# Kernel optimization log

Hardware: AMD Instinct MI355X
Metric: run time of the kernel (lower is better)

Reference implementation:

```python
import jax, jax.numpy as jnp
import numpy as np

N = 100000
C = 32            # channels per degree (shape_in == shape_out == 32)
NI = C * C        # flattened Gram-matrix size = n_input = n_hidden
LN_EPS = 1e-5
SLOPE = 0.01      # LeakyReLU default negative slope


def _ln(x, g, b):
    mu = jnp.mean(x, axis=-1, keepdims=True)
    var = jnp.var(x, axis=-1, keepdims=True)  # biased, matches torch LayerNorm
    return (x - mu) * jax.lax.rsqrt(var + LN_EPS) * g + b


def _lrelu(x):
    return jnp.where(x >= 0, x, SLOPE * x)


def _gal(v, g1, b1, w1, g2, b2, w2, bias2):
    # v: [N, ch_in, m]
    n, ci, _ = v.shape
    dot = jnp.einsum('nac,nbc->nab', v, v).reshape(n, ci * ci)  # Gram matrix
    dot = jnp.sign(dot) * jnp.maximum(jnp.abs(dot), 1e-12)
    h = _lrelu(_ln(dot, g1, b1)) @ w1.T           # [N, ch_in*ch_out]
    h = _lrelu(_ln(h, g2, b2)) @ w2.T + bias2      # [N, ch_in*ch_out]
    attn = jax.nn.softmax(h.reshape(n, -1, ci), axis=-1)  # [N, ch_out, ch_in]
    return jnp.einsum('nab,nbc->nac', attn, v)     # [N, ch_out, m]


def _mk_type_params(key):
    ks = jax.random.split(key, 3)
    bound = np.sqrt(6.0 / NI)  # kaiming_uniform_, fan_in=NI
    return dict(
        ln1_g=jnp.ones((NI,), jnp.float32),
        ln1_b=jnp.zeros((NI,), jnp.float32),
        w1=jax.random.uniform(ks[0], (NI, NI), jnp.float32, -bound, bound),
        ln2_g=jnp.ones((NI,), jnp.float32),
        ln2_b=jnp.zeros((NI,), jnp.float32),
        w2=jax.random.uniform(ks[1], (NI, NI), jnp.float32, -bound, bound),
        b2=jax.random.uniform(ks[2], (NI,), jnp.float32, -1.0 / C, 1.0 / C),
    )


def setup_inputs():
    key = jax.random.key(0)
    k0, k1, kp0, kp1 = jax.random.split(key, 4)
    d = {
        'f0': jax.random.normal(k0, (N, C, 1), jnp.float32),
        'f1': jax.random.normal(k1, (N, C, 3), jnp.float32),
    }
    for tag, kk in (('0', kp0), ('1', kp1)):
        p = _mk_type_params(kk)
        for name, val in p.items():
            d[f'{name}_{tag}'] = val
    return d


def reference(f0, f1,
              ln1_g_0, ln1_b_0, w1_0, ln2_g_0, ln2_b_0, w2_0, b2_0,
              ln1_g_1, ln1_b_1, w1_1, ln2_g_1, ln2_b_1, w2_1, b2_1):
    out0 = _gal(f0, ln1_g_0, ln1_b_0, w1_0, ln2_g_0, ln2_b_0, w2_0, b2_0)
    out1 = _gal(f1, ln1_g_1, ln1_b_1, w1_1, ln2_g_1, ln2_b_1, w2_1, b2_1)
    return (out0, out1)
```

## Files before the change

### kernel.cpp

```cpp
#include <hip/hip_runtime.h>

#define NN     100000
#define NB     1563
#define LN_EPS 1e-5f
#define SLOPE  0.01f

typedef __bf16 bf16x8 __attribute__((ext_vector_type(8)));
typedef float  f32x4  __attribute__((ext_vector_type(4)));
typedef unsigned short u16;
typedef unsigned int   u32;

union Pack8 { uint4 u4; bf16x8 bf; u16 s[8]; };

__device__ __forceinline__ u16 f2bf(float x){
    u32 b = __float_as_uint(x);
    b += 0x7fffu + ((b >> 16) & 1u);
    return (u16)(b >> 16);
}
__device__ __forceinline__ float bf2f(u32 s){
    return __uint_as_float(s << 16);
}

__global__ __launch_bounds__(1024) void prep_weights(
    const float* __restrict__ wa, const float* __restrict__ wb,
    const float* __restrict__ wc, const float* __restrict__ wd,
    u16* __restrict__ dst)
{
    int m = blockIdx.y;
    const float* src = (m==0)? wa : (m==1)? wb : (m==2)? wc : wd;
    u16* d = dst + (size_t)m * (1024u*1024u);
    int tid = blockIdx.x * blockDim.x + threadIdx.x;
    int sub = tid & 3;
    int row = (tid >> 2) & 1023;
    int kb  = tid >> 12;
    const float4* s4 = (const float4*)(src + row*1024 + kb*32 + sub*8);
    float4 a = s4[0], b = s4[1];
    Pack8 p;
    p.s[0]=f2bf(a.x); p.s[1]=f2bf(a.y); p.s[2]=f2bf(a.z); p.s[3]=f2bf(a.w);
    p.s[4]=f2bf(b.x); p.s[5]=f2bf(b.y); p.s[6]=f2bf(b.z); p.s[7]=f2bf(b.w);
    ((uint4*)d)[(kb*1024 + row)*4 + sub] = p.u4;
}

__device__ __forceinline__ void gemm_quad(
    const u16* __restrict__ Wp, const u16* xs,
    int wv, int lane15, int q, f32x4 acc[4][4])
{
    const uint4* bA = (const uint4*)Wp + (wv*32 + lane15)*4 + q;
    const uint4* bB = (const uint4*)Wp + ((wv+16)*32 + lane15)*4 + q;
    const uint4* ab = (const uint4*)xs + q*64 + lane15;
    #pragma unroll
    for (int ct=0; ct<4; ++ct)
      #pragma unroll
      for (int rt=0; rt<4; ++rt)
        acc[ct][rt] = (f32x4){0.f,0.f,0.f,0.f};
    #pragma unroll 2
    for (int ks=0; ks<32; ++ks){
        Pack8 b0, b1, b2, b3, a0, a1, a2, a3;
        b0.u4 = bA[ks*4096];
        b1.u4 = bA[ks*4096 + 64];
        b2.u4 = bB[ks*4096];
        b3.u4 = bB[ks*4096 + 64];
        a0.u4 = ab[ks*256];
        a1.u4 = ab[ks*256 + 16];
        a2.u4 = ab[ks*256 + 32];
        a3.u4 = ab[ks*256 + 48];
        acc[0][0] = __builtin_amdgcn_mfma_f32_16x16x32_bf16(a0.bf, b0.bf, acc[0][0], 0,0,0);
        acc[0][1] = __builtin_amdgcn_mfma_f32_16x16x32_bf16(a1.bf, b0.bf, acc[0][1], 0,0,0);
        acc[0][2] = __builtin_amdgcn_mfma_f32_16x16x32_bf16(a2.bf, b0.bf, acc[0][2], 0,0,0);
        acc[0][3] = __builtin_amdgcn_mfma_f32_16x16x32_bf16(a3.bf, b0.bf, acc[0][3], 0,0,0);
        acc[1][0] = __builtin_amdgcn_mfma_f32_16x16x32_bf16(a0.bf, b1.bf, acc[1][0], 0,0,0);
        acc[1][1] = __builtin_amdgcn_mfma_f32_16x16x32_bf16(a1.bf, b1.bf, acc[1][1], 0,0,0);
        acc[1][2] = __builtin_amdgcn_mfma_f32_16x16x32_bf16(a2.bf, b1.bf, acc[1][2], 0,0,0);
        acc[1][3] = __builtin_amdgcn_mfma_f32_16x16x32_bf16(a3.bf, b1.bf, acc[1][3], 0,0,0);
        acc[2][0] = __builtin_amdgcn_mfma_f32_16x16x32_bf16(a0.bf, b2.bf, acc[2][0], 0,0,0);
        acc[2][1] = __builtin_amdgcn_mfma_f32_16x16x32_bf16(a1.bf, b2.bf, acc[2][1], 0,0,0);
        acc[2][2] = __builtin_amdgcn_mfma_f32_16x16x32_bf16(a2.bf, b2.bf, acc[2][2], 0,0,0);
        acc[2][3] = __builtin_amdgcn_mfma_f32_16x16x32_bf16(a3.bf, b2.bf, acc[2][3], 0,0,0);
        acc[3][0] = __builtin_amdgcn_mfma_f32_16x16x32_bf16(a0.bf, b3.bf, acc[3][0], 0,0,0);
        acc[3][1] = __builtin_amdgcn_mfma_f32_16x16x32_bf16(a1.bf, b3.bf, acc[3][1], 0,0,0);
        acc[3][2] = __builtin_amdgcn_mfma_f32_16x16x32_bf16(a2.bf, b3.bf, acc[3][2], 0,0,0);
        acc[3][3] = __builtin_amdgcn_mfma_f32_16x16x32_bf16(a3.bf, b3.bf, acc[3][3], 0,0,0);
    }
}

template<int MDIM>
__global__ __launch_bounds__(1024, 4) void gal_fused(
    const float* __restrict__ f,
    const float* __restrict__ ln1g, const float* __restrict__ ln1b,
    const float* __restrict__ ln2g, const float* __restrict__ ln2b,
    const float* __restrict__ b2,
    const u16* __restrict__ Wp1, const u16* __restrict__ Wp2,
    float* __restrict__ outp)
{
    extern __shared__ char smem[];
    constexpr int VSTR = 32*MDIM + 4;
    constexpr int SBS  = 64*32 + 4;
    u16*   xs    = (u16*)smem;
    float* sbuf  = (float*)smem;
    float* vbuf  = (float*)smem + 32832;
    float* stats = (float*)smem + 32832 + 64*VSTR;

    const int tid    = threadIdx.x;
    const int lane   = tid & 63;
    const int wv     = tid >> 6;
    const int lane15 = lane & 15;
    const int q      = lane >> 4;
    const int node0  = blockIdx.x * 64;

    if (tid < 128) stats[tid] = 0.f;
    {
        const int gbase = node0*32*MDIM;
        for (int i = tid; i < 64*32*MDIM; i += 1024){
            int nd = i / (32*MDIM);
            int r  = i - nd*(32*MDIM);
            float val = (gbase + i < NN*32*MDIM) ? f[gbase + i] : 0.f;
            vbuf[nd*VSTR + r] = val;
        }
    }
    __syncthreads();

    {
        const int n = tid >> 4;
        const int j = tid & 15;
        const float* vn = vbuf + n*VSTR;
        float va[2][MDIM];
        #pragma unroll
        for (int c=0;c<MDIM;++c){ va[0][c]=vn[(j*2)*MDIM+c]; va[1][c]=vn[(j*2+1)*MDIM+c]; }
        float sum=0.f, ssum=0.f;
        #pragma unroll
        for (int b=0;b<32;++b){
            float d0=0.f, d1=0.f;
            #pragma unroll
            for (int c=0;c<MDIM;++c){ float vb = vn[b*MDIM+c]; d0 += va[0][c]*vb; d1 += va[1][c]*vb; }
            sum += d0+d1; ssum += d0*d0 + d1*d1;
        }
        #pragma unroll
        for (int st=1; st<16; st<<=1){ sum += __shfl_xor(sum, st); ssum += __shfl_xor(ssum, st); }
        float mu   = sum * (1.f/1024.f);
        float rstd = rsqrtf(ssum*(1.f/1024.f) - mu*mu + LN_EPS);
        #pragma unroll
        for (int jb=0;jb<8;++jb){
            Pack8 p;
            const int ai = jb >> 2;
            #pragma unroll
            for (int l=0;l<8;++l){
                int b = (jb*8+l) & 31;
                float d = 0.f;
                #pragma unroll
                for (int c=0;c<MDIM;++c) d += va[ai][c]*vn[b*MDIM+c];
                int k = j*64 + jb*8 + l;
                float x = (d - mu)*rstd*ln1g[k] + ln1b[k];
                x = (x >= 0.f)? x : SLOPE*x;
                p.s[l] = f2bf(x);
            }
            ((uint4*)xs)[(j*8+jb)*64 + n] = p.u4;
        }
    }
    __syncthreads();

    u32 h1pk[4][4][2];
    {
        f32x4 acc[4][4];
        gemm_quad(Wp1, xs, wv, lane15, q, acc);
        float p_[16], pp_[16];
        #pragma unroll
        for (int idx=0; idx<16; ++idx){
            int rt = idx>>2, rr = idx&3;
            float s=0.f, s2=0.f;
            #pragma unroll
            for (int ct=0; ct<4; ++ct){
                float h = acc[ct][rt][rr];
                s += h; s2 += h*h;
            }
            p_[idx] = s; pp_[idx] = s2;
        }
        #pragma unroll
        for (int m=8; m>=1; m>>=1){
            const bool hi = (lane15 & m) != 0;
            #pragma unroll
            for (int i=0; i<m; ++i){
                float sp = hi ? p_[i]  : p_[i+m];
                float kp = hi ? p_[i+m]  : p_[i];
                p_[i]  = kp + __shfl_xor(sp, m);
                float sq = hi ? pp_[i] : pp_[i+m];
                float kq = hi ? pp_[i+m] : pp_[i];
                pp_[i] = kq + __shfl_xor(sq, m);
            }
        }
        {
            int nd = (lane15>>2)*16 + q*4 + (lane15&3);
            atomicAdd(&stats[2*nd],   p_[0]);
            atomicAdd(&stats[2*nd+1], pp_[0]);
        }
        #pragma unroll
        for (int ct=0; ct<4; ++ct)
          #pragma unroll
          for (int rt=0; rt<4; ++rt){
            h1pk[ct][rt][0] = (u32)f2bf(acc[ct][rt][0]) | ((u32)f2bf(acc[ct][rt][1])<<16);
            h1pk[ct][rt][1] = (u32)f2bf(acc[ct][rt][2]) | ((u32)f2bf(acc[ct][rt][3])<<16);
          }
    }
    __syncthreads();

    {
        float g2c[4], b2c[4];
        #pragma unroll
        for (int ct=0; ct<4; ++ct){
            int col = (wv + (ct>>1)*16)*32 + (ct&1)*16 + lane15;
            g2c[ct] = ln2g[col];
            b2c[ct] = ln2b[col];
        }
        #pragma unroll
        for (int rt=0; rt<4; ++rt)
          #pragma unroll
          for (int rr=0; rr<4; ++rr){
            int nd = rt*16 + q*4 + rr;
            float mu   = stats[2*nd]*(1.f/1024.f);
            float rstd = rsqrtf(stats[2*nd+1]*(1.f/1024.f) - mu*mu + LN_EPS);
            #pragma unroll
            for (int ct=0; ct<4; ++ct){
                u32 u = h1pk[ct][rt][rr>>1];
                float h = bf2f((rr&1)? (u>>16) : (u & 0xffffu));
                float x = (h - mu)*rstd*g2c[ct] + b2c[ct];
                x = (x >= 0.f)? x : SLOPE*x;
                int col = (wv + (ct>>1)*16)*32 + (ct&1)*16 + lane15;
                xs[(col>>3)*512 + nd*8 + (col&7)] = f2bf(x);
            }
          }
    }
    __syncthreads();

    {
        f32x4 acc[4][4];
        gemm_quad(Wp2, xs, wv, lane15, q, acc);
        float bias[4];
        #pragma unroll
        for (int ct=0; ct<4; ++ct)
            bias[ct] = b2[(wv + (ct>>1)*16)*32 + (ct&1)*16 + lane15];
        __syncthreads();

        #pragma unroll
        for (int si=0; si<2; ++si){
            #pragma unroll
            for (int ctl=0; ctl<2; ++ctl){
                const int ct = si*2 + ctl;
                #pragma unroll
                for (int rt=0; rt<4; ++rt)
                  #pragma unroll
                  for (int rr=0; rr<4; ++rr){
                    int nd = rt*16 + q*4 + rr;
                    sbuf[wv*SBS + nd*32 + ctl*16 + lane15] = acc[ct][rt][rr] + bias[ct];
                  }
            }
            __syncthreads();
            {
                const int nd  = tid >> 4;
                const int a15 = tid & 15;
                const float* hp = sbuf + a15*SBS + nd*32;
                float e[32];
                #pragma unroll
                for (int r=0;r<8;++r){
                    float4 v4 = ((const float4*)hp)[r];
                    e[4*r]=v4.x; e[4*r+1]=v4.y; e[4*r+2]=v4.z; e[4*r+3]=v4.w;
                }
                float mx = e[0];
                #pragma unroll
                for (int b=1;b<32;++b) mx = fmaxf(mx, e[b]);
                float sm = 0.f;
                #pragma unroll
                for (int b=0;b<32;++b){ e[b] = __expf(e[b]-mx); sm += e[b]; }
                float inv = 1.f / sm;
                float oacc[MDIM];
                #pragma unroll
                for (int c=0;c<MDIM;++c) oacc[c]=0.f;
                const float4* vr = (const float4*)(vbuf + nd*VSTR);
                #pragma unroll
                for (int r=0; r<8*MDIM; ++r){
                    float4 v4 = vr[r];
                    #pragma unroll
                    for (int t=0;t<4;++t){
                        const int fi = 4*r+t;
                        const int b  = fi/MDIM;
                        const int c  = fi - b*MDIM;
                        float comp = (t==0)?v4.x:(t==1)?v4.y:(t==2)?v4.z:v4.w;
                        oacc[c] += e[b]*comp;
                    }
                }
                int ng = node0 + nd;
                if (ng < NN){
                    #pragma unroll
                    for (int c=0;c<MDIM;++c)
                        outp[((size_t)ng*32 + a15 + si*16)*MDIM + c] = oacc[c]*inv;
                }
            }
            if (si==0) __syncthreads();
        }
    }
}

extern "C" void kernel_launch(void* const* d_in, const int* in_sizes, int n_in,
                              void* d_out, int out_size, void* d_ws, size_t ws_size,
                              hipStream_t stream)
{
    const float* f0    = (const float*)d_in[0];
    const float* f1    = (const float*)d_in[1];
    const float* ln1g0 = (const float*)d_in[2];
    const float* ln1b0 = (const float*)d_in[3];
    const float* w1_0  = (const float*)d_in[4];
    const float* ln2g0 = (const float*)d_in[5];
    const float* ln2b0 = (const float*)d_in[6];
    const float* w2_0  = (const float*)d_in[7];
    const float* b2_0  = (const float*)d_in[8];
    const float* ln1g1 = (const float*)d_in[9];
    const float* ln1b1 = (const float*)d_in[10];
    const float* w1_1  = (const float*)d_in[11];
    const float* ln2g1 = (const float*)d_in[12];
    const float* ln2b1 = (const float*)d_in[13];
    const float* w2_1  = (const float*)d_in[14];
    const float* b2_1  = (const float*)d_in[15];
    float* out = (float*)d_out;
    u16* wp = (u16*)d_ws;

    const int smem1 = (32832 + 64*(32*1+4) + 128)*4;
    const int smem3 = (32832 + 64*(32*3+4) + 128)*4;
    (void)hipFuncSetAttribute(reinterpret_cast<const void*>(&gal_fused<1>),
                              hipFuncAttributeMaxDynamicSharedMemorySize, smem1);
    (void)hipFuncSetAttribute(reinterpret_cast<const void*>(&gal_fused<3>),
                              hipFuncAttributeMaxDynamicSharedMemorySize, smem3);

    prep_weights<<<dim3(128,4), 1024, 0, stream>>>(w1_0, w2_0, w1_1, w2_1, wp);
    gal_fused<1><<<NB, 1024, smem1, stream>>>(f0, ln1g0, ln1b0, ln2g0, ln2b0, b2_0,
                                              wp,            wp + 1048576, out);
    gal_fused<3><<<NB, 1024, smem3, stream>>>(f1, ln1g1, ln1b1, ln2g1, ln2b1, b2_1,
                                              wp + 2097152,  wp + 3145728, out + (size_t)NN*32);
}
```

Measured before the change: 1.392 ms.

## Prefetch weight fragments in GEMM loop, vectorize loads, keep fp32 hidden activations

The GEMM inner loop now software-prefetches the next k-step's weight fragments into registers and unrolls by 4, aiming to hide global-load latency behind the MFMA issue. The input staging loop uses float4 loads, and the LayerNorm-1 gamma/beta are read as float4 vectors instead of scalars. The first GEMM's fp32 accumulators are kept live through the second LayerNorm instead of being packed to bf16 and unpacked, which removes conversion work and a rounding step. In exchange register pressure rises, which risks spills at 1024 threads per block, and the prefetch wraps around to issue one redundant load at the end.

```diff
diff --git a/kernel.cpp b/kernel.cpp
--- a/kernel.cpp
+++ b/kernel.cpp
@@ -16,9 +16,6 @@
     u32 b = __float_as_uint(x);
     b += 0x7fffu + ((b >> 16) & 1u);
     return (u16)(b >> 16);
-}
-__device__ __forceinline__ float bf2f(u32 s){
-    return __uint_as_float(s << 16);
 }
 
 __global__ __launch_bounds__(1024) void prep_weights(
@@ -53,13 +50,16 @@
       #pragma unroll
       for (int rt=0; rt<4; ++rt)
         acc[ct][rt] = (f32x4){0.f,0.f,0.f,0.f};
-    #pragma unroll 2
+    uint4 nb0 = bA[0], nb1 = bA[64], nb2 = bB[0], nb3 = bB[64];
+    #pragma unroll 4
     for (int ks=0; ks<32; ++ks){
         Pack8 b0, b1, b2, b3, a0, a1, a2, a3;
-        b0.u4 = bA[ks*4096];
-        b1.u4 = bA[ks*4096 + 64];
-        b2.u4 = bB[ks*4096];
-        b3.u4 = bB[ks*4096 + 64];
+        b0.u4 = nb0; b1.u4 = nb1; b2.u4 = nb2; b3.u4 = nb3;
+        const int kn = (ks+1) & 31;
+        nb0 = bA[kn*4096];
+        nb1 = bA[kn*4096 + 64];
+        nb2 = bB[kn*4096];
+        nb3 = bB[kn*4096 + 64];
         a0.u4 = ab[ks*256];
         a1.u4 = ab[ks*256 + 16];
         a2.u4 = ab[ks*256 + 32];
@@ -109,12 +109,15 @@
 
     if (tid < 128) stats[tid] = 0.f;
     {
-        const int gbase = node0*32*MDIM;
-        for (int i = tid; i < 64*32*MDIM; i += 1024){
-            int nd = i / (32*MDIM);
-            int r  = i - nd*(32*MDIM);
-            float val = (gbase + i < NN*32*MDIM) ? f[gbase + i] : 0.f;
-            vbuf[nd*VSTR + r] = val;
+        float4* vbuf4 = (float4*)vbuf;
+        const int gv4  = node0*8*MDIM;
+        const int lim4 = NN*8*MDIM;
+        for (int i = tid; i < 64*8*MDIM; i += 1024){
+            int nd = i / (8*MDIM);
+            int r4 = i - nd*(8*MDIM);
+            float4 val = (gv4 + i < lim4) ? ((const float4*)f)[gv4 + i]
+                                          : (float4){0.f,0.f,0.f,0.f};
+            vbuf4[nd*(VSTR/4) + r4] = val;
         }
     }
     __syncthreads();
@@ -140,6 +143,13 @@
         float rstd = rsqrtf(ssum*(1.f/1024.f) - mu*mu + LN_EPS);
         #pragma unroll
         for (int jb=0;jb<8;++jb){
+            const int k0 = j*64 + jb*8;
+            float4 ga = ((const float4*)(ln1g + k0))[0];
+            float4 gb = ((const float4*)(ln1g + k0))[1];
+            float4 ba = ((const float4*)(ln1b + k0))[0];
+            float4 bb = ((const float4*)(ln1b + k0))[1];
+            float gg[8] = {ga.x,ga.y,ga.z,ga.w,gb.x,gb.y,gb.z,gb.w};
+            float bbv[8] = {ba.x,ba.y,ba.z,ba.w,bb.x,bb.y,bb.z,bb.w};
             Pack8 p;
             const int ai = jb >> 2;
             #pragma unroll
@@ -148,8 +158,7 @@
                 float d = 0.f;
                 #pragma unroll
                 for (int c=0;c<MDIM;++c) d += va[ai][c]*vn[b*MDIM+c];
-                int k = j*64 + jb*8 + l;
-                float x = (d - mu)*rstd*ln1g[k] + ln1b[k];
+                float x = (d - mu)*rstd*gg[l] + bbv[l];
                 x = (x >= 0.f)? x : SLOPE*x;
                 p.s[l] = f2bf(x);
             }
@@ -158,51 +167,41 @@
     }
     __syncthreads();
 
-    u32 h1pk[4][4][2];
     {
         f32x4 acc[4][4];
         gemm_quad(Wp1, xs, wv, lane15, q, acc);
-        float p_[16], pp_[16];
-        #pragma unroll
-        for (int idx=0; idx<16; ++idx){
-            int rt = idx>>2, rr = idx&3;
-            float s=0.f, s2=0.f;
-            #pragma unroll
-            for (int ct=0; ct<4; ++ct){
-                float h = acc[ct][rt][rr];
-                s += h; s2 += h*h;
-            }
-            p_[idx] = s; pp_[idx] = s2;
-        }
-        #pragma unroll
-        for (int m=8; m>=1; m>>=1){
-            const bool hi = (lane15 & m) != 0;
-            #pragma unroll
-            for (int i=0; i<m; ++i){
-                float sp = hi ? p_[i]  : p_[i+m];
-                float kp = hi ? p_[i+m]  : p_[i];
-                p_[i]  = kp + __shfl_xor(sp, m);
-                float sq = hi ? pp_[i] : pp_[i+m];
-                float kq = hi ? pp_[i+m] : pp_[i];
-                pp_[i] = kq + __shfl_xor(sq, m);
-            }
-        }
         {
+            float p_[16], pp_[16];
+            #pragma unroll
+            for (int idx=0; idx<16; ++idx){
+                int rt = idx>>2, rr = idx&3;
+                float s=0.f, s2=0.f;
+                #pragma unroll
+                for (int ct=0; ct<4; ++ct){
+                    float h = acc[ct][rt][rr];
+                    s += h; s2 += h*h;
+                }
+                p_[idx] = s; pp_[idx] = s2;
+            }
+            #pragma unroll
+            for (int m=8; m>=1; m>>=1){
+                const bool hi = (lane15 & m) != 0;
+                #pragma unroll
+                for (int i=0; i<m; ++i){
+                    float sp = hi ? p_[i]  : p_[i+m];
+                    float kp = hi ? p_[i+m]  : p_[i];
+                    p_[i]  = kp + __shfl_xor(sp, m);
+                    float sq = hi ? pp_[i] : pp_[i+m];
+                    float kq = hi ? pp_[i+m] : pp_[i];
+                    pp_[i] = kq + __shfl_xor(sq, m);
+                }
+            }
             int nd = (lane15>>2)*16 + q*4 + (lane15&3);
             atomicAdd(&stats[2*nd],   p_[0]);
             atomicAdd(&stats[2*nd+1], pp_[0]);
         }
-        #pragma unroll
-        for (int ct=0; ct<4; ++ct)
-          #pragma unroll
-          for (int rt=0; rt<4; ++rt){
-            h1pk[ct][rt][0] = (u32)f2bf(acc[ct][rt][0]) | ((u32)f2bf(acc[ct][rt][1])<<16);
-            h1pk[ct][rt][1] = (u32)f2bf(acc[ct][rt][2]) | ((u32)f2bf(acc[ct][rt][3])<<16);
-          }
-    }
-    __syncthreads();
-
-    {
+        __syncthreads();
+
         float g2c[4], b2c[4];
         #pragma unroll
         for (int ct=0; ct<4; ++ct){
@@ -219,8 +218,7 @@
             float rstd = rsqrtf(stats[2*nd+1]*(1.f/1024.f) - mu*mu + LN_EPS);
             #pragma unroll
             for (int ct=0; ct<4; ++ct){
-                u32 u = h1pk[ct][rt][rr>>1];
-                float h = bf2f((rr&1)? (u>>16) : (u & 0xffffu));
+                float h = acc[ct][rt][rr];
                 float x = (h - mu)*rstd*g2c[ct] + b2c[ct];
                 x = (x >= 0.f)? x : SLOPE*x;
                 int col = (wv + (ct>>1)*16)*32 + (ct&1)*16 + lane15;
```

After: 1.512 ms. 8.6% more time.
